# Performance work log

Hardware: AMD Instinct MI355X
Metric: run time of the kernel (lower is better)

## Reference

```python
import jax, jax.numpy as jnp
import numpy as np

D_MODEL = 1024
N_HEADS = 16
N_LAYERS = 2
D_FF = 4 * D_MODEL
CAUSAL_WINDOW = 6
LN_EPS = 1e-5
NEG = -1e30  # effectively -inf for fp32 softmax, grad-safe


def setup_inputs() -> dict:
    key = jax.random.key(0)
    ks = jax.random.split(key, 16)
    B, T, D, L, F = 4, 2048, D_MODEL, N_LAYERS, D_FF
    s = 0.02  # small init so deep residual stack stays well-scaled
    inp = {
        "x": jax.random.normal(ks[0], (B, T, D), jnp.float32),
        "key_padding_mask": jnp.zeros((B, T), jnp.bool_),
        "w_qkv": jax.random.normal(ks[1], (L, 3 * D, D), jnp.float32) * s,
        "b_qkv": jnp.zeros((L, 3 * D), jnp.float32),
        "w_out": jax.random.normal(ks[2], (L, D, D), jnp.float32) * s,
        "b_out": jnp.zeros((L, D), jnp.float32),
        "ln1_g": jnp.ones((L, D), jnp.float32),
        "ln1_b": jnp.zeros((L, D), jnp.float32),
        "ln2_g": jnp.ones((L, D), jnp.float32),
        "ln2_b": jnp.zeros((L, D), jnp.float32),
        "w1": jax.random.normal(ks[3], (L, F, D), jnp.float32) * s,
        "b1": jnp.zeros((L, F), jnp.float32),
        "w2": jax.random.normal(ks[4], (L, D, F), jnp.float32) * s,
        "b2": jnp.zeros((L, D), jnp.float32),
    }
    return inp


def _ln(x, g, b):
    mu = jnp.mean(x, axis=-1, keepdims=True)
    var = jnp.mean(jnp.square(x - mu), axis=-1, keepdims=True)
    return (x - mu) * jax.lax.rsqrt(var + LN_EPS) * g + b


def _forward(x, key_padding_mask, w_qkv, b_qkv, w_out, b_out,
             ln1_g, ln1_b, ln2_g, ln2_b, w1, b1, w2, b2):
    B, T, D = x.shape
    H = N_HEADS
    hd = D // H
    idx = jnp.arange(T)
    band = jnp.where(jnp.abs(idx[None, :] - idx[:, None]) > CAUSAL_WINDOW, NEG, 0.0)  # (T,T)
    kpm = jnp.where(key_padding_mask[:, None, None, :], NEG, 0.0)  # (B,1,1,T)
    add_mask = band[None, None] + kpm  # (B,1,T,T) broadcast over heads

    h = x
    for l in range(N_LAYERS):
        # --- self-attention sublayer (pre-norm) ---
        hn = _ln(h, ln1_g[l], ln1_b[l])
        qkv = hn @ w_qkv[l].T + b_qkv[l]  # (B,T,3D)
        q, k, v = jnp.split(qkv, 3, axis=-1)
        q = q.reshape(B, T, H, hd).transpose(0, 2, 1, 3)
        k = k.reshape(B, T, H, hd).transpose(0, 2, 1, 3)
        v = v.reshape(B, T, H, hd).transpose(0, 2, 1, 3)
        scores = jnp.einsum('bhqd,bhkd->bhqk', q, k) / jnp.sqrt(jnp.float32(hd))
        attn = jax.nn.softmax(scores + add_mask, axis=-1)
        o = jnp.einsum('bhqk,bhkd->bhqd', attn, v)
        o = o.transpose(0, 2, 1, 3).reshape(B, T, D)
        h = h + (o @ w_out[l].T + b_out[l])
        # --- feedforward sublayer (pre-norm) ---
        hn2 = _ln(h, ln2_g[l], ln2_b[l])
        ff = jax.nn.gelu(hn2 @ w1[l].T + b1[l], approximate=False) @ w2[l].T + b2[l]
        h = h + ff
    return h


def reference(x, key_padding_mask, w_qkv, b_qkv, w_out, b_out,
              ln1_g, ln1_b, ln2_g, ln2_b, w1, b1, w2, b2):
    return _forward(x, key_padding_mask, w_qkv, b_qkv, w_out, b_out,
                    ln1_g, ln1_b, ln2_g, ln2_b, w1, b1, w2, b2)
```

## Files before the change

### kernel.cpp

```cpp
#include <hip/hip_runtime.h>
#include <cstdint>
#include <cstddef>

typedef unsigned short u16;
typedef __attribute__((ext_vector_type(8))) short bf16x8;
typedef __attribute__((ext_vector_type(4))) float f32x4;

namespace {
constexpr int BATCH = 4;
constexpr int SEQ   = 2048;
constexpr int DM    = 1024;
constexpr int NH    = 16;
constexpr int HDIM  = 64;
constexpr int NL    = 2;
constexpr int DFF   = 4096;
constexpr int MROWS = BATCH * SEQ;
constexpr int WIN   = 6;

constexpr size_t OFF_H    = 0;
constexpr size_t OFF_ABUF = (size_t)32 << 20;
constexpr size_t OFF_BBUF = (size_t)48 << 20;
constexpr size_t OFF_WBUF = (size_t)112 << 20;
constexpr size_t WS_REQUIRED = (size_t)120 << 20;
}

static __device__ __forceinline__ float b2f(u16 u) {
    return __builtin_bit_cast(float, (unsigned int)u << 16);
}
static __device__ __forceinline__ u16 f2b(float f) {
    unsigned int u = __builtin_bit_cast(unsigned int, f);
    u += 0x7FFFu + ((u >> 16) & 1u);
    return (u16)(u >> 16);
}

__global__ __launch_bounds__(256) void fallback_k(const float* __restrict__ x,
                                                  float* __restrict__ out, int n) {
    int i = blockIdx.x * 256 + threadIdx.x;
    if (i < n) out[i] = x[i];
}

__global__ __launch_bounds__(256) void f2b_k(const float* __restrict__ in,
                                             u16* __restrict__ out, int n4) {
    int i = blockIdx.x * 256 + threadIdx.x;
    if (i < n4) {
        float4 v = ((const float4*)in)[i];
        unsigned int lo = (unsigned int)f2b(v.x) | ((unsigned int)f2b(v.y) << 16);
        unsigned int hi = (unsigned int)f2b(v.z) | ((unsigned int)f2b(v.w) << 16);
        ((uint2*)out)[i] = make_uint2(lo, hi);
    }
}

__global__ __launch_bounds__(256) void ln_k(const float* __restrict__ x,
                                            const float* __restrict__ g,
                                            const float* __restrict__ b,
                                            u16* __restrict__ out) {
    __shared__ float red[8];
    const int row = blockIdx.x;
    const float4 v = ((const float4*)(x + (size_t)row * DM))[threadIdx.x];
    float s1 = v.x + v.y + v.z + v.w;
    float s2 = v.x * v.x + v.y * v.y + v.z * v.z + v.w * v.w;
    #pragma unroll
    for (int o = 32; o; o >>= 1) {
        s1 += __shfl_xor(s1, o);
        s2 += __shfl_xor(s2, o);
    }
    const int wid = threadIdx.x >> 6, lane = threadIdx.x & 63;
    if (lane == 0) { red[wid] = s1; red[4 + wid] = s2; }
    __syncthreads();
    s1 = red[0] + red[1] + red[2] + red[3];
    s2 = red[4] + red[5] + red[6] + red[7];
    const float mu  = s1 * (1.0f / DM);
    const float var = s2 * (1.0f / DM) - mu * mu;
    const float inv = rsqrtf(var + 1e-5f);
    const float4 gg = ((const float4*)g)[threadIdx.x];
    const float4 bb = ((const float4*)b)[threadIdx.x];
    unsigned int lo = (unsigned int)f2b((v.x - mu) * inv * gg.x + bb.x)
                    | ((unsigned int)f2b((v.y - mu) * inv * gg.y + bb.y) << 16);
    unsigned int hi = (unsigned int)f2b((v.z - mu) * inv * gg.z + bb.z)
                    | ((unsigned int)f2b((v.w - mu) * inv * gg.w + bb.w) << 16);
    ((uint2*)(out + (size_t)row * DM))[threadIdx.x] = make_uint2(lo, hi);
}

__global__ __launch_bounds__(64, 2) void attn_k(const u16* __restrict__ qkv,
                                                const unsigned char* __restrict__ kpm,
                                                u16* __restrict__ out) {
    __shared__ u16 kv[76 * 68];
    __shared__ float p_s[13 * 64];
    const int lane = threadIdx.x;
    const int bid  = blockIdx.x;
    const int qt = bid & (SEQ / 64 - 1);
    const int h  = (bid >> 5) & (NH - 1);
    const int b  = bid >> 9;
    const int t0 = qt * 64;
    const int t  = t0 + lane;
    const size_t rstride = 3 * DM;

    const u16* qbase = qkv + ((size_t)b * SEQ + t) * rstride + h * HDIM;
    float q[64];
    #pragma unroll
    for (int c = 0; c < 8; ++c) {
        uint4 v = *(const uint4*)(qbase + c * 8);
        unsigned int w0 = v.x, w1 = v.y, w2 = v.z, w3 = v.w;
        q[c*8+0] = b2f((u16)(w0 & 0xffff)) * 0.125f;
        q[c*8+1] = b2f((u16)(w0 >> 16))    * 0.125f;
        q[c*8+2] = b2f((u16)(w1 & 0xffff)) * 0.125f;
        q[c*8+3] = b2f((u16)(w1 >> 16))    * 0.125f;
        q[c*8+4] = b2f((u16)(w2 & 0xffff)) * 0.125f;
        q[c*8+5] = b2f((u16)(w2 >> 16))    * 0.125f;
        q[c*8+6] = b2f((u16)(w3 & 0xffff)) * 0.125f;
        q[c*8+7] = b2f((u16)(w3 >> 16))    * 0.125f;
    }

    auto stage = [&](int which) {
        const u16* src0 = qkv + ((size_t)b * SEQ) * rstride + which * DM + h * HDIM;
        #pragma unroll
        for (int it = 0; it < 10; ++it) {
            int g = it * 64 + lane;
            if (g < 608) {
                int row = g >> 3, cc = g & 7;
                int j = t0 - 6 + row;
                j = min(max(j, 0), SEQ - 1);
                uint4 v = *(const uint4*)(src0 + (size_t)j * rstride + cc * 8);
                *(uint2*)(kv + row * 68 + cc * 8)     = make_uint2(v.x, v.y);
                *(uint2*)(kv + row * 68 + cc * 8 + 4) = make_uint2(v.z, v.w);
            }
        }
    };

    stage(1);
    __syncthreads();
    for (int u = 0; u < 13; ++u) {
        const u16* krow = kv + (lane + u) * 68;
        float s = 0.f;
        #pragma unroll
        for (int c = 0; c < 16; ++c) {
            uint2 v = *(const uint2*)(krow + c * 4);
            s += q[c*4+0] * b2f((u16)(v.x & 0xffff));
            s += q[c*4+1] * b2f((u16)(v.x >> 16));
            s += q[c*4+2] * b2f((u16)(v.y & 0xffff));
            s += q[c*4+3] * b2f((u16)(v.y >> 16));
        }
        int j = t - WIN + u;
        bool ok = (j >= 0) && (j < SEQ);
        if (ok && kpm[b * SEQ + j]) ok = false;
        p_s[u * 64 + lane] = ok ? s : -1e30f;
    }

    float mx = -1e30f;
    for (int u = 0; u < 13; ++u) mx = fmaxf(mx, p_s[u * 64 + lane]);
    float den = 0.f;
    for (int u = 0; u < 13; ++u) {
        float e = __expf(p_s[u * 64 + lane] - mx);
        p_s[u * 64 + lane] = e;
        den += e;
    }
    const float inv = 1.0f / den;

    __syncthreads();
    stage(2);
    __syncthreads();
    u16* orow = out + ((size_t)b * SEQ + t) * DM + h * HDIM;
    #pragma unroll
    for (int dc = 0; dc < 4; ++dc) {
        float o[16] = {};
        for (int u = 0; u < 13; ++u) {
            const float p = p_s[u * 64 + lane];
            const u16* vrow = kv + (lane + u) * 68 + dc * 16;
            #pragma unroll
            for (int c = 0; c < 4; ++c) {
                uint2 v = *(const uint2*)(vrow + c * 4);
                o[c*4+0] += p * b2f((u16)(v.x & 0xffff));
                o[c*4+1] += p * b2f((u16)(v.x >> 16));
                o[c*4+2] += p * b2f((u16)(v.y & 0xffff));
                o[c*4+3] += p * b2f((u16)(v.y >> 16));
            }
        }
        unsigned int pk[8];
        #pragma unroll
        for (int i = 0; i < 8; ++i)
            pk[i] = (unsigned int)f2b(o[2*i] * inv)
                  | ((unsigned int)f2b(o[2*i+1] * inv) << 16);
        *(uint4*)(orow + dc * 16)     = make_uint4(pk[0], pk[1], pk[2], pk[3]);
        *(uint4*)(orow + dc * 16 + 8) = make_uint4(pk[4], pk[5], pk[6], pk[7]);
    }
}

template <int EPI>
__global__ __launch_bounds__(256) void gemm_nt(const u16* __restrict__ A,
                                               const u16* __restrict__ Bw,
                                               const float* __restrict__ bias,
                                               const float* __restrict__ res,
                                               float* __restrict__ outf,
                                               u16* __restrict__ outb,
                                               int M, int N, int K) {
    __shared__ u16 As[128 * 64];
    __shared__ u16 Bs[128 * 64];
    const int tid  = threadIdx.x;
    const int lane = tid & 63;
    const int wid  = tid >> 6;
    const int wm = wid >> 1, wn = wid & 1;
    const int r = lane & 15, quad = lane >> 4;
    const int row0a = blockIdx.y * 128;
    const int row0b = blockIdx.x * 128;

    f32x4 acc[4][4] = {};

    for (int k0 = 0; k0 < K; k0 += 64) {
        #pragma unroll
        for (int s = 0; s < 4; ++s) {
            int e8  = s * 256 + tid;
            int rw  = e8 >> 3;
            int sl  = e8 & 7;
            int ssl = sl ^ (rw & 7);
            const u16* ga = A  + (size_t)(row0a + rw) * K + k0 + ssl * 8;
            const u16* gb = Bw + (size_t)(row0b + rw) * K + k0 + ssl * 8;
            u16* la = As + (size_t)(s * 256 + wid * 64) * 8;
            u16* lb = Bs + (size_t)(s * 256 + wid * 64) * 8;
            __builtin_amdgcn_global_load_lds((const __attribute__((address_space(1))) void*)ga,
                                             (__attribute__((address_space(3))) void*)la, 16, 0, 0);
            __builtin_amdgcn_global_load_lds((const __attribute__((address_space(1))) void*)gb,
                                             (__attribute__((address_space(3))) void*)lb, 16, 0, 0);
        }
        asm volatile("s_waitcnt vmcnt(0)" ::: "memory");
        __syncthreads();

        #pragma unroll
        for (int kk = 0; kk < 2; ++kk) {
            bf16x8 af[4], bfg[4];
            #pragma unroll
            for (int mi = 0; mi < 4; ++mi) {
                int rw = wm * 64 + mi * 16 + r;
                int sl = (kk * 4 + quad) ^ (rw & 7);
                af[mi] = *(const bf16x8*)(As + rw * 64 + sl * 8);
            }
            #pragma unroll
            for (int ni = 0; ni < 4; ++ni) {
                int rw = wn * 64 + ni * 16 + r;
                int sl = (kk * 4 + quad) ^ (rw & 7);
                bfg[ni] = *(const bf16x8*)(Bs + rw * 64 + sl * 8);
            }
            #pragma unroll
            for (int mi = 0; mi < 4; ++mi)
                #pragma unroll
                for (int ni = 0; ni < 4; ++ni)
                    acc[mi][ni] = __builtin_amdgcn_mfma_f32_16x16x32_bf16(
                        af[mi], bfg[ni], acc[mi][ni], 0, 0, 0);
        }
        __syncthreads();
    }

    const int mbase = row0a + wm * 64 + quad * 4;
    const int nbase = row0b + wn * 64 + r;
    #pragma unroll
    for (int mi = 0; mi < 4; ++mi) {
        #pragma unroll
        for (int ni = 0; ni < 4; ++ni) {
            const int n = nbase + ni * 16;
            const float bv = bias[n];
            #pragma unroll
            for (int j = 0; j < 4; ++j) {
                const int m = mbase + mi * 16 + j;
                float c = acc[mi][ni][j] + bv;
                const size_t idx = (size_t)m * N + n;
                if constexpr (EPI == 1) {
                    c = 0.5f * c * (1.0f + erff(c * 0.70710678118654752f));
                }
                if constexpr (EPI == 2) {
                    outf[idx] = c + res[idx];
                } else {
                    outb[idx] = f2b(c);
                }
            }
        }
    }
}

extern "C" void kernel_launch(void* const* d_in, const int* in_sizes, int n_in,
                              void* d_out, int out_size, void* d_ws, size_t ws_size,
                              hipStream_t stream) {
    const float* x     = (const float*)d_in[0];
    const unsigned char* kpm = (const unsigned char*)d_in[1];
    const float* w_qkv = (const float*)d_in[2];
    const float* b_qkv = (const float*)d_in[3];
    const float* w_out = (const float*)d_in[4];
    const float* b_out = (const float*)d_in[5];
    const float* ln1_g = (const float*)d_in[6];
    const float* ln1_b = (const float*)d_in[7];
    const float* ln2_g = (const float*)d_in[8];
    const float* ln2_b = (const float*)d_in[9];
    const float* w1    = (const float*)d_in[10];
    const float* b1    = (const float*)d_in[11];
    const float* w2    = (const float*)d_in[12];
    const float* b2    = (const float*)d_in[13];
    float* out = (float*)d_out;

    if (ws_size < WS_REQUIRED) {
        int n = out_size;
        fallback_k<<<(n + 255) / 256, 256, 0, stream>>>(x, out, n);
        return;
    }

    char* ws = (char*)d_ws;
    float* h    = (float*)(ws + OFF_H);
    u16*  Abuf  = (u16*)(ws + OFF_ABUF);
    u16*  Bbuf  = (u16*)(ws + OFF_BBUF);
    u16*  Wbuf  = (u16*)(ws + OFF_WBUF);

    auto conv = [&](const float* src, size_t n) {
        int n4 = (int)(n / 4);
        f2b_k<<<(n4 + 255) / 256, 256, 0, stream>>>(src, Wbuf, n4);
    };

    hipMemcpyAsync(h, x, (size_t)MROWS * DM * sizeof(float),
                   hipMemcpyDeviceToDevice, stream);

    for (int l = 0; l < NL; ++l) {
        ln_k<<<MROWS, 256, 0, stream>>>(h, ln1_g + (size_t)l * DM, ln1_b + (size_t)l * DM, Abuf);
        conv(w_qkv + (size_t)l * 3 * DM * DM, (size_t)3 * DM * DM);
        gemm_nt<0><<<dim3(3 * DM / 128, MROWS / 128), 256, 0, stream>>>(
            Abuf, Wbuf, b_qkv + (size_t)l * 3 * DM,
            nullptr, nullptr, Bbuf, MROWS, 3 * DM, DM);
        attn_k<<<BATCH * NH * (SEQ / 64), 64, 0, stream>>>(Bbuf, kpm, Abuf);
        conv(w_out + (size_t)l * DM * DM, (size_t)DM * DM);
        gemm_nt<2><<<dim3(DM / 128, MROWS / 128), 256, 0, stream>>>(
            Abuf, Wbuf, b_out + (size_t)l * DM,
            h, h, nullptr, MROWS, DM, DM);
        ln_k<<<MROWS, 256, 0, stream>>>(h, ln2_g + (size_t)l * DM, ln2_b + (size_t)l * DM, Abuf);
        conv(w1 + (size_t)l * DFF * DM, (size_t)DFF * DM);
        gemm_nt<1><<<dim3(DFF / 128, MROWS / 128), 256, 0, stream>>>(
            Abuf, Wbuf, b1 + (size_t)l * DFF,
            nullptr, nullptr, Bbuf, MROWS, DFF, DM);
        conv(w2 + (size_t)l * DM * DFF, (size_t)DM * DFF);
        float* ff2out = (l == NL - 1) ? out : h;
        gemm_nt<2><<<dim3(DM / 128, MROWS / 128), 256, 0, stream>>>(
            Bbuf, Wbuf, b2 + (size_t)l * DM,
            h, ff2out, nullptr, MROWS, DM, DFF);
    }
}
```

Before: 864.4 us.

## Triple-buffer GEMM loads with 256x128 tiles and 8-wave ping-pong MFMA scheduling

The bf16 GEMM is restructured to use 512 threads and 256x128 output tiles. Global-to-LDS loads go into a three-slot ring buffer, prefetched two K-steps ahead, in place of the single-buffer load, wait, compute loop. Each K-step is split into two halves separated by barriers, with s_setprio raised around the MFMA bursts so waves interleave LDS reads and matrix math. The intent is to hide global load latency and cut per-tile barrier stalls. The cost is more LDS per block (three 48 KB slots) and fewer blocks in the grid, and the wm mapping must cover 256 rows correctly.

```diff
diff --git a/kernel.cpp b/kernel.cpp
--- a/kernel.cpp
+++ b/kernel.cpp
@@ -22,6 +22,8 @@
 constexpr size_t OFF_BBUF = (size_t)48 << 20;
 constexpr size_t OFF_WBUF = (size_t)112 << 20;
 constexpr size_t WS_REQUIRED = (size_t)120 << 20;
+
+constexpr int SLOT = 384 * 64;
 }
 
 static __device__ __forceinline__ float b2f(u16 u) {
@@ -186,67 +188,118 @@
 }
 
 template <int EPI>
-__global__ __launch_bounds__(256) void gemm_nt(const u16* __restrict__ A,
-                                               const u16* __restrict__ Bw,
-                                               const float* __restrict__ bias,
-                                               const float* __restrict__ res,
-                                               float* __restrict__ outf,
-                                               u16* __restrict__ outb,
-                                               int M, int N, int K) {
-    __shared__ u16 As[128 * 64];
-    __shared__ u16 Bs[128 * 64];
+__global__ __launch_bounds__(512, 2) void gemm_nt(const u16* __restrict__ A,
+                                                  const u16* __restrict__ Bw,
+                                                  const float* __restrict__ bias,
+                                                  const float* __restrict__ res,
+                                                  float* __restrict__ outf,
+                                                  u16* __restrict__ outb,
+                                                  int M, int N, int K) {
+    __shared__ u16 lds[3 * SLOT];
     const int tid  = threadIdx.x;
     const int lane = tid & 63;
     const int wid  = tid >> 6;
-    const int wm = wid >> 1, wn = wid & 1;
+    const int wm = wid >> 1;
+    const int wn = wid & 1;
     const int r = lane & 15, quad = lane >> 4;
-    const int row0a = blockIdx.y * 128;
+    const int row0a = blockIdx.y * 256;
     const int row0b = blockIdx.x * 128;
+    const int nt = K >> 6;
+
+    const u16* gsrc[6];
+    int dofs[6];
+    #pragma unroll
+    for (int s4 = 0; s4 < 4; ++s4) {
+        int e8 = s4 * 512 + tid;
+        int rw = e8 >> 3, sl = e8 & 7, ssl = sl ^ (rw & 7);
+        gsrc[s4] = A + (size_t)(row0a + rw) * K + ssl * 8;
+        dofs[s4] = e8 * 8;
+    }
+    #pragma unroll
+    for (int s4 = 0; s4 < 2; ++s4) {
+        int e8 = s4 * 512 + tid;
+        int rw = e8 >> 3, sl = e8 & 7, ssl = sl ^ (rw & 7);
+        gsrc[4 + s4] = Bw + (size_t)(row0b + rw) * K + ssl * 8;
+        dofs[4 + s4] = 256 * 64 + e8 * 8;
+    }
+    auto stage = [&](u16* base, int k0) {
+        #pragma unroll
+        for (int i = 0; i < 6; ++i)
+            __builtin_amdgcn_global_load_lds(
+                (const __attribute__((address_space(1))) void*)(gsrc[i] + k0),
+                (__attribute__((address_space(3))) void*)(base + dofs[i]), 16, 0, 0);
+    };
+
+    stage(lds, 0);
+    if (nt > 1) stage(lds + SLOT, 64);
+    if (nt > 2) asm volatile("s_waitcnt vmcnt(6)" ::: "memory");
+    else        asm volatile("s_waitcnt vmcnt(0)" ::: "memory");
+    __builtin_amdgcn_s_barrier();
 
     f32x4 acc[4][4] = {};
-
-    for (int k0 = 0; k0 < K; k0 += 64) {
-        #pragma unroll
-        for (int s = 0; s < 4; ++s) {
-            int e8  = s * 256 + tid;
-            int rw  = e8 >> 3;
-            int sl  = e8 & 7;
-            int ssl = sl ^ (rw & 7);
-            const u16* ga = A  + (size_t)(row0a + rw) * K + k0 + ssl * 8;
-            const u16* gb = Bw + (size_t)(row0b + rw) * K + k0 + ssl * 8;
-            u16* la = As + (size_t)(s * 256 + wid * 64) * 8;
-            u16* lb = Bs + (size_t)(s * 256 + wid * 64) * 8;
-            __builtin_amdgcn_global_load_lds((const __attribute__((address_space(1))) void*)ga,
-                                             (__attribute__((address_space(3))) void*)la, 16, 0, 0);
-            __builtin_amdgcn_global_load_lds((const __attribute__((address_space(1))) void*)gb,
-                                             (__attribute__((address_space(3))) void*)lb, 16, 0, 0);
-        }
-        asm volatile("s_waitcnt vmcnt(0)" ::: "memory");
-        __syncthreads();
-
+    int cur = 0, pre = 2, kpre = 128;
+    for (int t = 0; t < nt; ++t) {
+        const u16* As = lds + cur * SLOT;
+        const u16* Bs = As + 256 * 64;
+        const bool doPre = (t + 2 < nt);
+        if (doPre) stage(lds + pre * SLOT, kpre);
+
+        bf16x8 bfg[2][4], af[2][2];
         #pragma unroll
         for (int kk = 0; kk < 2; ++kk) {
-            bf16x8 af[4], bfg[4];
-            #pragma unroll
-            for (int mi = 0; mi < 4; ++mi) {
-                int rw = wm * 64 + mi * 16 + r;
-                int sl = (kk * 4 + quad) ^ (rw & 7);
-                af[mi] = *(const bf16x8*)(As + rw * 64 + sl * 8);
-            }
             #pragma unroll
             for (int ni = 0; ni < 4; ++ni) {
                 int rw = wn * 64 + ni * 16 + r;
                 int sl = (kk * 4 + quad) ^ (rw & 7);
-                bfg[ni] = *(const bf16x8*)(Bs + rw * 64 + sl * 8);
-            }
-            #pragma unroll
-            for (int mi = 0; mi < 4; ++mi)
+                bfg[kk][ni] = *(const bf16x8*)(Bs + rw * 64 + sl * 8);
+            }
+            #pragma unroll
+            for (int mi = 0; mi < 2; ++mi) {
+                int rw = wm * 64 + mi * 16 + r;
+                int sl = (kk * 4 + quad) ^ (rw & 7);
+                af[kk][mi] = *(const bf16x8*)(As + rw * 64 + sl * 8);
+            }
+        }
+        __builtin_amdgcn_s_barrier();
+        __builtin_amdgcn_s_setprio(1);
+        #pragma unroll
+        for (int mi = 0; mi < 2; ++mi)
+            #pragma unroll
+            for (int ni = 0; ni < 4; ++ni)
                 #pragma unroll
-                for (int ni = 0; ni < 4; ++ni)
+                for (int kk = 0; kk < 2; ++kk)
                     acc[mi][ni] = __builtin_amdgcn_mfma_f32_16x16x32_bf16(
-                        af[mi], bfg[ni], acc[mi][ni], 0, 0, 0);
-        }
-        __syncthreads();
+                        af[kk][mi], bfg[kk][ni], acc[mi][ni], 0, 0, 0);
+        __builtin_amdgcn_s_setprio(0);
+        __builtin_amdgcn_s_barrier();
+
+        bf16x8 af2[2][2];
+        #pragma unroll
+        for (int kk = 0; kk < 2; ++kk)
+            #pragma unroll
+            for (int mi = 0; mi < 2; ++mi) {
+                int rw = wm * 64 + (mi + 2) * 16 + r;
+                int sl = (kk * 4 + quad) ^ (rw & 7);
+                af2[kk][mi] = *(const bf16x8*)(As + rw * 64 + sl * 8);
+            }
+        __builtin_amdgcn_s_barrier();
+        __builtin_amdgcn_s_setprio(1);
+        #pragma unroll
+        for (int mi = 0; mi < 2; ++mi)
+            #pragma unroll
+            for (int ni = 0; ni < 4; ++ni)
+                #pragma unroll
+                for (int kk = 0; kk < 2; ++kk)
+                    acc[mi + 2][ni] = __builtin_amdgcn_mfma_f32_16x16x32_bf16(
+                        af2[kk][mi], bfg[kk][ni], acc[mi + 2][ni], 0, 0, 0);
+        __builtin_amdgcn_s_setprio(0);
+        if (doPre) asm volatile("s_waitcnt vmcnt(6)" ::: "memory");
+        else       asm volatile("s_waitcnt vmcnt(0)" ::: "memory");
+        __builtin_amdgcn_s_barrier();
+
+        cur = (cur == 2) ? 0 : cur + 1;
+        pre = (pre == 2) ? 0 : pre + 1;
+        kpre += 64;
     }
 
     const int mbase = row0a + wm * 64 + quad * 4;
@@ -317,22 +370,22 @@
     for (int l = 0; l < NL; ++l) {
         ln_k<<<MROWS, 256, 0, stream>>>(h, ln1_g + (size_t)l * DM, ln1_b + (size_t)l * DM, Abuf);
         conv(w_qkv + (size_t)l * 3 * DM * DM, (size_t)3 * DM * DM);
-        gemm_nt<0><<<dim3(3 * DM / 128, MROWS / 128), 256, 0, stream>>>(
+        gemm_nt<0><<<dim3(3 * DM / 128, MROWS / 256), 512, 0, stream>>>(
             Abuf, Wbuf, b_qkv + (size_t)l * 3 * DM,
             nullptr, nullptr, Bbuf, MROWS, 3 * DM, DM);
         attn_k<<<BATCH * NH * (SEQ / 64), 64, 0, stream>>>(Bbuf, kpm, Abuf);
         conv(w_out + (size_t)l * DM * DM, (size_t)DM * DM);
-        gemm_nt<2><<<dim3(DM / 128, MROWS / 128), 256, 0, stream>>>(
+        gemm_nt<2><<<dim3(DM / 128, MROWS / 256), 512, 0, stream>>>(
             Abuf, Wbuf, b_out + (size_t)l * DM,
             h, h, nullptr, MROWS, DM, DM);
         ln_k<<<MROWS, 256, 0, stream>>>(h, ln2_g + (size_t)l * DM, ln2_b + (size_t)l * DM, Abuf);
         conv(w1 + (size_t)l * DFF * DM, (size_t)DFF * DM);
-        gemm_nt<1><<<dim3(DFF / 128, MROWS / 128), 256, 0, stream>>>(
+        gemm_nt<1><<<dim3(DFF / 128, MROWS / 256), 512, 0, stream>>>(
             Abuf, Wbuf, b1 + (size_t)l * DFF,
             nullptr, nullptr, Bbuf, MROWS, DFF, DM);
         conv(w2 + (size_t)l * DM * DFF, (size_t)DM * DFF);
         float* ff2out = (l == NL - 1) ? out : h;
-        gemm_nt<2><<<dim3(DM / 128, MROWS / 128), 256, 0, stream>>>(
+        gemm_nt<2><<<dim3(DM / 128, MROWS / 256), 512, 0, stream>>>(
             Bbuf, Wbuf, b2 + (size_t)l * DM,
             h, ff2out, nullptr, MROWS, DM, DFF);
     }
```

New measurement: 871.9 us. Within noise of the previous version (+0.9%).

## Double-buffer GEMM LDS tiles so global loads overlap MFMA compute

Applied to the files above, without the earlier changes.

Splits the GEMM shared memory into two slots. The next K-tile is issued with global_load_lds into the idle slot while MFMAs run on the current one, which hides global-memory latency behind compute. Global source pointers and LDS offsets are precomputed once instead of per iteration, and launch bounds now request two blocks per CU. In exchange the kernel uses twice as much LDS, and occupancy depends on the hardware fitting two 64 KB blocks per CU.

```diff
diff --git a/kernel.cpp b/kernel.cpp
--- a/kernel.cpp
+++ b/kernel.cpp
@@ -22,6 +22,8 @@
 constexpr size_t OFF_BBUF = (size_t)48 << 20;
 constexpr size_t OFF_WBUF = (size_t)112 << 20;
 constexpr size_t WS_REQUIRED = (size_t)120 << 20;
+
+constexpr int SLOT = 256 * 64;
 }
 
 static __device__ __forceinline__ float b2f(u16 u) {
@@ -186,15 +188,14 @@
 }
 
 template <int EPI>
-__global__ __launch_bounds__(256) void gemm_nt(const u16* __restrict__ A,
-                                               const u16* __restrict__ Bw,
-                                               const float* __restrict__ bias,
-                                               const float* __restrict__ res,
-                                               float* __restrict__ outf,
-                                               u16* __restrict__ outb,
-                                               int M, int N, int K) {
-    __shared__ u16 As[128 * 64];
-    __shared__ u16 Bs[128 * 64];
+__global__ __launch_bounds__(256, 2) void gemm_nt(const u16* __restrict__ A,
+                                                  const u16* __restrict__ Bw,
+                                                  const float* __restrict__ bias,
+                                                  const float* __restrict__ res,
+                                                  float* __restrict__ outf,
+                                                  u16* __restrict__ outb,
+                                                  int M, int N, int K) {
+    __shared__ u16 lds[2 * SLOT];
     const int tid  = threadIdx.x;
     const int lane = tid & 63;
     const int wid  = tid >> 6;
@@ -202,27 +203,42 @@
     const int r = lane & 15, quad = lane >> 4;
     const int row0a = blockIdx.y * 128;
     const int row0b = blockIdx.x * 128;
+    const int nt = K >> 6;
+
+    const u16* gsrc[8];
+    int dofs[8];
+    #pragma unroll
+    for (int s4 = 0; s4 < 4; ++s4) {
+        int e8 = s4 * 256 + tid;
+        int rw = e8 >> 3, sl = e8 & 7, ssl = sl ^ (rw & 7);
+        gsrc[s4] = A + (size_t)(row0a + rw) * K + ssl * 8;
+        dofs[s4] = e8 * 8;
+    }
+    #pragma unroll
+    for (int s4 = 0; s4 < 4; ++s4) {
+        int e8 = s4 * 256 + tid;
+        int rw = e8 >> 3, sl = e8 & 7, ssl = sl ^ (rw & 7);
+        gsrc[4 + s4] = Bw + (size_t)(row0b + rw) * K + ssl * 8;
+        dofs[4 + s4] = 128 * 64 + e8 * 8;
+    }
+    auto stage = [&](u16* base, int k0) {
+        #pragma unroll
+        for (int i = 0; i < 8; ++i)
+            __builtin_amdgcn_global_load_lds(
+                (const __attribute__((address_space(1))) void*)(gsrc[i] + k0),
+                (__attribute__((address_space(3))) void*)(base + dofs[i]), 16, 0, 0);
+    };
+
+    stage(lds, 0);
+    asm volatile("s_waitcnt vmcnt(0)" ::: "memory");
+    __builtin_amdgcn_s_barrier();
 
     f32x4 acc[4][4] = {};
-
-    for (int k0 = 0; k0 < K; k0 += 64) {
-        #pragma unroll
-        for (int s = 0; s < 4; ++s) {
-            int e8  = s * 256 + tid;
-            int rw  = e8 >> 3;
-            int sl  = e8 & 7;
-            int ssl = sl ^ (rw & 7);
-            const u16* ga = A  + (size_t)(row0a + rw) * K + k0 + ssl * 8;
-            const u16* gb = Bw + (size_t)(row0b + rw) * K + k0 + ssl * 8;
-            u16* la = As + (size_t)(s * 256 + wid * 64) * 8;
-            u16* lb = Bs + (size_t)(s * 256 + wid * 64) * 8;
-            __builtin_amdgcn_global_load_lds((const __attribute__((address_space(1))) void*)ga,
-                                             (__attribute__((address_space(3))) void*)la, 16, 0, 0);
-            __builtin_amdgcn_global_load_lds((const __attribute__((address_space(1))) void*)gb,
-                                             (__attribute__((address_space(3))) void*)lb, 16, 0, 0);
-        }
-        asm volatile("s_waitcnt vmcnt(0)" ::: "memory");
-        __syncthreads();
+    int cur = 0;
+    for (int t = 0; t < nt; ++t) {
+        const u16* As = lds + cur * SLOT;
+        const u16* Bs = As + 128 * 64;
+        if (t + 1 < nt) stage(lds + (cur ^ 1) * SLOT, (t + 1) * 64);
 
         #pragma unroll
         for (int kk = 0; kk < 2; ++kk) {
@@ -246,7 +262,9 @@
                     acc[mi][ni] = __builtin_amdgcn_mfma_f32_16x16x32_bf16(
                         af[mi], bfg[ni], acc[mi][ni], 0, 0, 0);
         }
-        __syncthreads();
+        asm volatile("s_waitcnt vmcnt(0)" ::: "memory");
+        __builtin_amdgcn_s_barrier();
+        cur ^= 1;
     }
 
     const int mbase = row0a + wm * 64 + quad * 4;
```

After: 829.6 us. -4.0%, faster.
